# Optimization experiments

Measured on AMD Instinct MI355X. Metric: run time of the kernel, lower is better.

The kernel has to match this reference:

```python
import jax, jax.numpy as jnp
import numpy as np

N = 100000          # item_nums (nodes)
E = 3200000         # edges
D = 64              # embedding dim
MASK_DEPTH = 2      # configs['model']['mask_depth']
PATH_PROB = 0.5     # configs['model']['path_prob']
NUM_CAND = 1024     # configs['model']['num_mask_cand']
EPS_DIV = 1e-8
EPS_NORM = 1e-12


def setup_inputs() -> dict:
    key = jax.random.key(0)
    k1, k2, k3, k4 = jax.random.split(key, 4)
    edge_rows = jax.random.randint(k1, (E,), 0, N, dtype=jnp.int32)
    edge_cols = jax.random.randint(k2, (E,), 0, N, dtype=jnp.int32)
    edge_vals = jax.random.uniform(k3, (E,), dtype=jnp.float32)
    embeds = jax.random.normal(k4, (N, D), dtype=jnp.float32)
    return {"edge_rows": edge_rows, "edge_cols": edge_cols,
            "edge_vals": edge_vals, "embeds": embeds}


def _l2norm(x):
    # torch F.normalize(p=2, dim=1)
    n = jnp.sqrt(jnp.sum(x * x, axis=-1, keepdims=True))
    return x / jnp.maximum(n, EPS_NORM)


def reference(edge_rows, edge_cols, edge_vals, embeds):
    def spmm(vals, x):  # adj @ x with adj in COO form; x: [N, d]
        return jax.ops.segment_sum(vals[:, None] * x[edge_cols], edge_rows,
                                   num_segments=N)

    def rowsum(vals):   # t.sparse.sum(adj, dim=-1) -> [N, 1]
        return jax.ops.segment_sum(vals, edge_rows, num_segments=N)[:, None]

    key = jax.random.key(42)
    vals = edge_vals

    order = rowsum(vals)
    fst = spmm(vals, embeds) - embeds            # fstEmbeds
    emb_sum, num_sum = fst, order                # running sum of emb/num lists
    emb_prev, num_prev = fst, order

    for i in range(MASK_DEPTH):
        key, kd = jax.random.split(key)
        keep = PATH_PROB ** (i + 1)
        # sparse_dropout: keep edge with prob `keep`, values NOT rescaled.
        # Dropping edges == zeroing their values for all subsequent spmm.
        mask = jnp.floor(jax.random.uniform(kd, (E,)) + keep)
        vals = vals * mask
        emb_new = spmm(vals, emb_prev) - emb_prev - order * emb_prev
        num_new = spmm(vals, num_prev) - num_prev - order
        order = rowsum(vals)
        emb_sum = emb_sum + emb_new
        num_sum = num_sum + num_new
        emb_prev, num_prev = emb_new, num_new

    subgraph = _l2norm(emb_sum / (num_sum + EPS_DIV))
    embeds_n = _l2norm(embeds)
    scores = jnp.sum(subgraph * embeds_n, axis=-1)   # [N]

    # make_noise: Gumbel noise -log(-log(U))
    key, kn = jax.random.split(key)
    u = jax.random.uniform(kn, (N,))
    scores = scores + (-jnp.log(-jnp.log(u)))

    _, candidates = jax.lax.top_k(scores, NUM_CAND)
    return scores, candidates
```

## Files before the change

kernel.cpp:

```cpp
#include <hip/hip_runtime.h>
#include <hip/hip_bf16.h>
#include <stdint.h>
#include <stddef.h>

#define NN 100000
#define NE 3200000
#define NCAND 1024
#define SCAN_BLOCKS 98
#define NB 391
#define CAP 10240
#define TILE 4096
#define NA_CAP 1700000
#define NB_CAP 500000

__host__ __device__ inline void tf2x32(uint32_t k0, uint32_t k1,
                                       uint32_t x0, uint32_t x1,
                                       uint32_t& y0, uint32_t& y1) {
  uint32_t ks2 = k0 ^ k1 ^ 0x1BD11BDAu;
  x0 += k0; x1 += k1;
#define TFR(r) { x0 += x1; x1 = (x1 << (r)) | (x1 >> (32 - (r))); x1 ^= x0; }
  TFR(13) TFR(15) TFR(26) TFR(6)
  x0 += k1;  x1 += ks2 + 1u;
  TFR(17) TFR(29) TFR(16) TFR(24)
  x0 += ks2; x1 += k0 + 2u;
  TFR(13) TFR(15) TFR(26) TFR(6)
  x0 += k0;  x1 += k1 + 3u;
  TFR(17) TFR(29) TFR(16) TFR(24)
  x0 += k1;  x1 += ks2 + 4u;
  TFR(13) TFR(15) TFR(26) TFR(6)
  x0 += ks2; x1 += k0 + 5u;
#undef TFR
  y0 = x0; y1 = x1;
}

__device__ inline float u01_from_key(uint32_t ka, uint32_t kb, uint32_t idx) {
  uint32_t y0, y1; tf2x32(ka, kb, 0u, idx, y0, y1);
  uint32_t bits = y0 ^ y1;
  return __uint_as_float((bits >> 9) | 0x3F800000u) - 1.0f;
}

__device__ inline float np_tree64(float w) {
#pragma clang fp contract(off)
  float acc = w;
  acc = acc + __shfl_down(w, 8);
  acc = acc + __shfl_down(w, 16);
  acc = acc + __shfl_down(w, 24);
  acc = acc + __shfl_down(w, 32);
  acc = acc + __shfl_down(w, 40);
  acc = acc + __shfl_down(w, 48);
  acc = acc + __shfl_down(w, 56);
  float u = acc + __shfl_xor(acc, 1);
  float v = u + __shfl_xor(u, 2);
  float f = v + __shfl_xor(v, 4);
  return __shfl(f, 0);
}

__global__ void __launch_bounds__(256) k_bucketA(const int* __restrict__ rows,
    const int* __restrict__ cols, const float* __restrict__ vals,
    uint32_t* __restrict__ bcur, uint32_t* __restrict__ bbufE,
    uint32_t* __restrict__ bbufC, float* __restrict__ bbufV,
    uint32_t kd0a, uint32_t kd0b, uint32_t kd1a, uint32_t kd1b) {
  __shared__ uint32_t cnt[NB], cnt2[NB], gbase[NB];
  __shared__ uint32_t pref[NB + 1];
  __shared__ uint32_t stageE[TILE];
  __shared__ uint32_t stageC[TILE];
  __shared__ float    stageV[TILE];
  __shared__ uint16_t stageB[TILE];
  int tid = threadIdx.x;
  int base_e = blockIdx.x * TILE;
  int vcnt = NE - base_e; if (vcnt > TILE) vcnt = TILE;
  for (int j = tid; j < NB; j += 256) { cnt[j] = 0u; cnt2[j] = 0u; }
  __syncthreads();
  for (int i = tid; i < vcnt; i += 256) {
    uint32_t r = (uint32_t)rows[base_e + i];
    atomicAdd(&cnt[r >> 8], 1u);
  }
  __syncthreads();
  if (tid == 0) {
    uint32_t run = 0;
    for (int j = 0; j < NB; j++) { pref[j] = run; run += cnt[j]; }
    pref[NB] = run;
  }
  for (int j = tid; j < NB; j += 256) gbase[j] = atomicAdd(&bcur[j], cnt[j]);
  __syncthreads();
  for (int i = tid; i < vcnt; i += 256) {
    uint32_t e = (uint32_t)(base_e + i);
    uint32_t r = (uint32_t)rows[e];
    uint32_t b = r >> 8, lr = r & 255u;
    uint32_t m0 = (u01_from_key(kd0a, kd0b, e) >= 0.5f) ? 1u : 0u;
    uint32_t m1 = (u01_from_key(kd1a, kd1b, e) >= 0.75f) ? 1u : 0u;
    uint32_t flags = (m0 << 30) | ((m0 & m1) << 31);
    uint32_t slot = pref[b] + atomicAdd(&cnt2[b], 1u);
    stageE[slot] = flags | (lr << 22) | e;
    stageC[slot] = (uint32_t)cols[e];
    stageV[slot] = vals[e];
    stageB[slot] = (uint16_t)b;
  }
  __syncthreads();
  for (int i = tid; i < vcnt; i += 256) {
    uint32_t b = stageB[i];
    size_t dst = (size_t)b * CAP + gbase[b] + ((uint32_t)i - pref[b]);
    bbufE[dst] = stageE[i];
    bbufC[dst] = stageC[i];
    bbufV[dst] = stageV[i];
  }
}

__global__ void __launch_bounds__(256) k_cnt(const uint32_t* __restrict__ bcur,
    const uint32_t* __restrict__ bbufE, uint32_t* __restrict__ total,
    uint32_t* __restrict__ totalA, uint32_t* __restrict__ totalB) {
  __shared__ uint32_t c0[256], c1[256], c2[256];
  int b = blockIdx.x, tid = threadIdx.x;
  c0[tid] = 0u; c1[tid] = 0u; c2[tid] = 0u;
  __syncthreads();
  uint32_t nE = bcur[b];
  for (uint32_t i = tid; i < nE; i += 256) {
    uint32_t pk = bbufE[(size_t)b * CAP + i];
    uint32_t lr = (pk >> 22) & 255u;
    atomicAdd(&c0[lr], 1u);
    if (pk & 0x40000000u) atomicAdd(&c1[lr], 1u);
    if (pk & 0x80000000u) atomicAdd(&c2[lr], 1u);
  }
  __syncthreads();
  int row = (b << 8) + tid;
  if (row < NN) { total[row] = c0[tid]; totalA[row] = c1[tid]; totalB[row] = c2[tid]; }
}

__global__ void k_scan1(const uint32_t* __restrict__ total, uint32_t* __restrict__ rstart,
                        uint32_t* __restrict__ bsum) {
  __shared__ uint32_t s[1024];
  int i = blockIdx.x * 1024 + threadIdx.x;
  uint32_t v = (i < NN) ? total[i] : 0u;
  s[threadIdx.x] = v; __syncthreads();
  for (int o = 1; o < 1024; o <<= 1) {
    uint32_t x = (threadIdx.x >= (unsigned)o) ? s[threadIdx.x - o] : 0u;
    __syncthreads();
    s[threadIdx.x] += x;
    __syncthreads();
  }
  if (i <= NN) rstart[i] = s[threadIdx.x] - v;
  if (threadIdx.x == 1023) bsum[blockIdx.x] = s[1023];
}

__global__ void k_scan2(uint32_t* __restrict__ bsum) {
  if (blockIdx.x == 0 && threadIdx.x == 0) {
    uint32_t run = 0;
    for (int b = 0; b < SCAN_BLOCKS; b++) { uint32_t t = bsum[b]; bsum[b] = run; run += t; }
  }
}

__global__ void k_scan3(uint32_t* __restrict__ rstart, const uint32_t* __restrict__ bsum) {
  int i = blockIdx.x * 1024 + threadIdx.x;
  if (i <= NN) rstart[i] += bsum[blockIdx.x];
}

__global__ void __launch_bounds__(256) k_buildB(const uint32_t* __restrict__ bbufE,
    const uint32_t* __restrict__ bbufC, const float* __restrict__ bbufV,
    const uint32_t* __restrict__ rstart, const uint32_t* __restrict__ rstartA,
    const uint32_t* __restrict__ rstartB,
    uint32_t* __restrict__ scol, float* __restrict__ v0s,
    uint32_t* __restrict__ scolA, float* __restrict__ vAa,
    uint32_t* __restrict__ scolB, float* __restrict__ vBa,
    float* __restrict__ order0, float* __restrict__ order1) {
#pragma clang fp contract(off)
  __shared__ uint32_t eidp[CAP];
  __shared__ uint16_t slot[CAP];
  __shared__ uint32_t rbase[257];
  __shared__ uint32_t rcur[256];
  int b = blockIdx.x, tid = threadIdx.x;
  int row0 = b << 8;
  int nrows = NN - row0; if (nrows > 256) nrows = 256;
  uint32_t base = rstart[row0];
  for (int j = tid; j <= nrows; j += 256) rbase[j] = rstart[row0 + j] - base;
  rcur[tid] = 0u;
  __syncthreads();
  uint32_t nE = rbase[nrows];
  const uint32_t* bE = bbufE + (size_t)b * CAP;
  const uint32_t* bC = bbufC + (size_t)b * CAP;
  const float*    bV = bbufV + (size_t)b * CAP;
  for (uint32_t i = tid; i < nE; i += 256) {
    uint32_t pk = bE[i];
    uint32_t lr = (pk >> 22) & 255u;
    uint32_t c = atomicAdd(&rcur[lr], 1u);
    uint32_t pos = rbase[lr] + c;
    eidp[pos] = pk;
    slot[pos] = (uint16_t)i;
  }
  __syncthreads();
  for (int lr = tid; lr < nrows; lr += 256) {
    uint32_t p0 = rbase[lr], p1 = rbase[lr + 1];
    for (uint32_t i = p0 + 1; i < p1; i++) {
      uint32_t key = eidp[i]; uint16_t ks = slot[i];
      uint32_t ke = key & 0x3FFFFFu;
      uint32_t j = i;
      while (j > p0 && (eidp[j - 1] & 0x3FFFFFu) > ke) {
        eidp[j] = eidp[j - 1]; slot[j] = slot[j - 1]; j--;
      }
      eidp[j] = key; slot[j] = ks;
    }
  }
  __syncthreads();
  for (uint32_t i = tid; i < nE; i += 256) {
    uint32_t s = slot[i];
    scol[(size_t)base + i] = bC[s];
    v0s[(size_t)base + i] = bV[s];
  }
  for (int lr = tid; lr < nrows; lr += 256) {
    uint32_t p0 = rbase[lr], p1 = rbase[lr + 1];
    uint32_t wA = rstartA[row0 + lr];
    uint32_t wB = rstartB[row0 + lr];
    float o0 = 0.0f, o1 = 0.0f;
    for (uint32_t p = p0; p < p1; p++) {
      uint32_t pk = eidp[p];
      uint32_t s = slot[p];
      float v = bV[s];
      o0 = o0 + v;
      if (pk & 0x40000000u) {
        o1 = o1 + v;
        uint32_t c = bC[s];
        scolA[wA] = c; vAa[wA] = v; wA++;
        if (pk & 0x80000000u) { scolB[wB] = c; vBa[wB] = v; wB++; }
      }
    }
    order0[row0 + lr] = o0; order1[row0 + lr] = o1;
  }
}

__global__ void __launch_bounds__(256) k_fst(const uint32_t* __restrict__ rp,
    const uint32_t* __restrict__ scol, const float* __restrict__ v0s,
    const float* __restrict__ emb, float* __restrict__ fst) {
#pragma clang fp contract(off)
  int r = blockIdx.x * 4 + (threadIdx.x >> 6);
  if (r >= NN) return;
  int d = threadIdx.x & 63;
  uint32_t p0 = rp[r], p1 = rp[r + 1];
  float acc = 0.0f;
  uint32_t p = p0;
  for (; p + 4 <= p1; p += 4) {
    uint32_t c0 = scol[p], c1 = scol[p + 1], c2 = scol[p + 2], c3 = scol[p + 3];
    float v0 = v0s[p], v1 = v0s[p + 1], v2 = v0s[p + 2], v3 = v0s[p + 3];
    float e0 = emb[(size_t)c0 * 64 + d];
    float e1 = emb[(size_t)c1 * 64 + d];
    float e2 = emb[(size_t)c2 * 64 + d];
    float e3 = emb[(size_t)c3 * 64 + d];
    acc = acc + v0 * e0; acc = acc + v1 * e1;
    acc = acc + v2 * e2; acc = acc + v3 * e3;
  }
  for (; p < p1; p++) acc = acc + v0s[p] * emb[(size_t)scol[p] * 64 + d];
  fst[(size_t)r * 64 + d] = acc - emb[(size_t)r * 64 + d];
}

__global__ void __launch_bounds__(256) k_numA(const uint32_t* __restrict__ rpA,
    const uint32_t* __restrict__ scolA, const float* __restrict__ vAa,
    const float* __restrict__ order0, float* __restrict__ num0) {
#pragma clang fp contract(off)
  int r = blockIdx.x * blockDim.x + threadIdx.x;
  if (r >= NN) return;
  uint32_t p0 = rpA[r], p1 = rpA[r + 1];
  float acc = 0.0f;
  uint32_t p = p0;
  for (; p + 4 <= p1; p += 4) {
    uint32_t c0 = scolA[p], c1 = scolA[p + 1], c2 = scolA[p + 2], c3 = scolA[p + 3];
    float v0 = vAa[p], v1 = vAa[p + 1], v2 = vAa[p + 2], v3 = vAa[p + 3];
    float o0 = order0[c0], o1 = order0[c1], o2 = order0[c2], o3 = order0[c3];
    acc = acc + v0 * o0; acc = acc + v1 * o1;
    acc = acc + v2 * o2; acc = acc + v3 * o3;
  }
  for (; p < p1; p++) acc = acc + vAa[p] * order0[scolA[p]];
  float o = order0[r];
  num0[r] = (acc - o) - o;
}

__global__ void __launch_bounds__(256) k_emb1(const uint32_t* __restrict__ rpA,
    const uint32_t* __restrict__ scolA, const float* __restrict__ vAa,
    const float* __restrict__ fst, const float* __restrict__ order0,
    float* __restrict__ emb1) {
#pragma clang fp contract(off)
  int r = blockIdx.x * 4 + (threadIdx.x >> 6);
  if (r >= NN) return;
  int d = threadIdx.x & 63;
  uint32_t p0 = rpA[r], p1 = rpA[r + 1];
  float acc = 0.0f;
  uint32_t p = p0;
  for (; p + 4 <= p1; p += 4) {
    uint32_t c0 = scolA[p], c1 = scolA[p + 1], c2 = scolA[p + 2], c3 = scolA[p + 3];
    float v0 = vAa[p], v1 = vAa[p + 1], v2 = vAa[p + 2], v3 = vAa[p + 3];
    float e0 = fst[(size_t)c0 * 64 + d];
    float e1 = fst[(size_t)c1 * 64 + d];
    float e2 = fst[(size_t)c2 * 64 + d];
    float e3 = fst[(size_t)c3 * 64 + d];
    acc = acc + v0 * e0; acc = acc + v1 * e1;
    acc = acc + v2 * e2; acc = acc + v3 * e3;
  }
  for (; p < p1; p++) acc = acc + vAa[p] * fst[(size_t)scolA[p] * 64 + d];
  size_t i = (size_t)r * 64 + d;
  float pr = fst[i];
  float t  = order0[r] * pr;
  emb1[i] = (acc - pr) - t;
}

__global__ void __launch_bounds__(256) k_numB(const uint32_t* __restrict__ rpB,
    const uint32_t* __restrict__ scolB, const float* __restrict__ vBa,
    const float* __restrict__ num0, const float* __restrict__ order0,
    const float* __restrict__ order1, float* __restrict__ num_sum) {
#pragma clang fp contract(off)
  int r = blockIdx.x * blockDim.x + threadIdx.x;
  if (r >= NN) return;
  uint32_t p0 = rpB[r], p1 = rpB[r + 1];
  float acc = 0.0f;
  for (uint32_t p = p0; p < p1; p++) acc = acc + vBa[p] * num0[scolB[p]];
  float n1 = (acc - num0[r]) - order1[r];
  num_sum[r] = (order0[r] + num0[r]) + n1;
}

__global__ void __launch_bounds__(256) k_emb2(const uint32_t* __restrict__ rpB,
    const uint32_t* __restrict__ scolB, const float* __restrict__ vBa,
    const float* __restrict__ emb1, const float* __restrict__ order1,
    float* __restrict__ fstsum) {
#pragma clang fp contract(off)
  int r = blockIdx.x * 4 + (threadIdx.x >> 6);
  if (r >= NN) return;
  int d = threadIdx.x & 63;
  uint32_t p0 = rpB[r], p1 = rpB[r + 1];
  float acc = 0.0f;
  uint32_t p = p0;
  for (; p + 4 <= p1; p += 4) {
    uint32_t c0 = scolB[p], c1 = scolB[p + 1], c2 = scolB[p + 2], c3 = scolB[p + 3];
    float v0 = vBa[p], v1 = vBa[p + 1], v2 = vBa[p + 2], v3 = vBa[p + 3];
    float e0 = emb1[(size_t)c0 * 64 + d];
    float e1 = emb1[(size_t)c1 * 64 + d];
    float e2 = emb1[(size_t)c2 * 64 + d];
    float e3 = emb1[(size_t)c3 * 64 + d];
    acc = acc + v0 * e0; acc = acc + v1 * e1;
    acc = acc + v2 * e2; acc = acc + v3 * e3;
  }
  for (; p < p1; p++) acc = acc + vBa[p] * emb1[(size_t)scolB[p] * 64 + d];
  size_t i = (size_t)r * 64 + d;
  float pr = emb1[i];
  float t  = order1[r] * pr;
  float e2v = (acc - pr) - t;
  fstsum[i] = (fstsum[i] + pr) + e2v;
}

__global__ void __launch_bounds__(256) k_scores(const float* __restrict__ esum,
    const float* __restrict__ num_sum, const float* __restrict__ emb,
    uint32_t* __restrict__ m_arr, float* __restrict__ out_scores,
    uint32_t kna, uint32_t knb) {
#pragma clang fp contract(off)
  int r = blockIdx.x * 4 + (threadIdx.x >> 6);
  if (r >= NN) return;
  int lane = threadIdx.x & 63;
  size_t ib = (size_t)r * 64 + lane;
  float denom = num_sum[r] + 1e-8f;
  float t = esum[ib] / denom;
  float S1 = np_tree64(t * t);
  float nn = fmaxf(sqrtf(S1), 1e-12f);
  t = t / nn;
  float e = emb[ib];
  float S2 = np_tree64(e * e);
  float mn = fmaxf(sqrtf(S2), 1e-12f);
  float s = np_tree64(t * (e / mn));
  if (lane == 0) {
    float u  = u01_from_key(kna, knb, (uint32_t)r);
    float l1 = (float)log((double)u);
    float l2 = (float)log((double)(-l1));
    s = s + (-l2);
    uint32_t bb = __float_as_uint(s);
    m_arr[r] = bb ^ (uint32_t)(((int32_t)bb >> 31) | (int32_t)0x80000000);
    out_scores[r] = s;
  }
}

__global__ void __launch_bounds__(1024)
k_topk(const uint32_t* __restrict__ m_arr, float* __restrict__ out) {
  __shared__ uint32_t hist[256];
  __shared__ uint32_t selp, need, ccnt;
  __shared__ unsigned long long cbuf[4096];
  int tid = threadIdx.x;
  if (tid == 0) { selp = 0u; need = NCAND; ccnt = 0u; }
  __syncthreads();
  for (int shift = 24; shift >= 0; shift -= 8) {
    if (tid < 256) hist[tid] = 0u;
    __syncthreads();
    uint32_t pref = selp;
    for (int i = tid; i < NN; i += 1024) {
      uint32_t m = m_arr[i];
      bool ok = (shift == 24) || ((m >> (shift + 8)) == pref);
      if (ok) atomicAdd(&hist[(m >> shift) & 255u], 1u);
    }
    __syncthreads();
    if (tid == 0) {
      uint32_t nd = need;
      int b;
      for (b = 255; b > 0; b--) {
        uint32_t c = hist[b];
        if (c < nd) nd -= c; else break;
      }
      selp = (pref << 8) | (uint32_t)b;
      need = nd;
    }
    __syncthreads();
  }
  uint32_t thr = selp;
  for (int i = tid; i < NN; i += 1024) {
    uint32_t m = m_arr[i];
    if (m >= thr) {
      uint32_t pos = atomicAdd(&ccnt, 1u);
      if (pos < 4096u)
        cbuf[pos] = ((unsigned long long)m << 32) | (uint32_t)(~(uint32_t)i);
    }
  }
  __syncthreads();
  uint32_t n = ccnt; if (n > 4096u) n = 4096u;
  for (int i = tid; i < 4096; i += 1024) if (i >= (int)n) cbuf[i] = 0ULL;
  __syncthreads();
  for (int k = 2; k <= 4096; k <<= 1) {
    for (int j = k >> 1; j > 0; j >>= 1) {
      for (int i = tid; i < 4096; i += 1024) {
        int ixj = i ^ j;
        if (ixj > i) {
          bool up = ((i & k) == 0);
          unsigned long long a = cbuf[i], b = cbuf[ixj];
          if ((a > b) == up) { cbuf[i] = b; cbuf[ixj] = a; }
        }
      }
      __syncthreads();
    }
  }
  for (int j = tid; j < NCAND; j += 1024) {
    unsigned long long key = cbuf[4095 - j];
    uint32_t idx = ~(uint32_t)(key & 0xFFFFFFFFull);
    out[j] = (float)idx;
  }
}

extern "C" void kernel_launch(void* const* d_in, const int* in_sizes, int n_in,
                              void* d_out, int out_size, void* d_ws, size_t ws_size,
                              hipStream_t stream) {
  (void)in_sizes; (void)n_in; (void)out_size; (void)ws_size;
  const int*   rows = (const int*)d_in[0];
  const int*   cols = (const int*)d_in[1];
  const float* vals = (const float*)d_in[2];
  const float* emb  = (const float*)d_in[3];
  float* out = (float*)d_out;

  char* w = (char*)d_ws;
  auto alloc = [&](size_t bytes) -> void* {
    void* p = (void*)w; w += (bytes + 255) & ~(size_t)255; return p;
  };
  uint32_t* bcur    = (uint32_t*)alloc((size_t)NB * 4);
  uint32_t* bbufE   = (uint32_t*)alloc((size_t)NB * CAP * 4);
  uint32_t* bbufC   = (uint32_t*)alloc((size_t)NB * CAP * 4);
  float*    bbufV   = (float*)   alloc((size_t)NB * CAP * 4);
  uint32_t* total   = (uint32_t*)alloc((size_t)NN * 4);
  uint32_t* totalA  = (uint32_t*)alloc((size_t)NN * 4);
  uint32_t* totalB  = (uint32_t*)alloc((size_t)NN * 4);
  uint32_t* rstart  = (uint32_t*)alloc((size_t)(NN + 1) * 4);
  uint32_t* rstartA = (uint32_t*)alloc((size_t)(NN + 1) * 4);
  uint32_t* rstartB = (uint32_t*)alloc((size_t)(NN + 1) * 4);
  uint32_t* bsum    = (uint32_t*)alloc((size_t)SCAN_BLOCKS * 4);
  uint32_t* scol    = (uint32_t*)alloc((size_t)NE * 4);
  float*    v0s     = (float*)   alloc((size_t)NE * 4);
  uint32_t* scolA   = (uint32_t*)alloc((size_t)NA_CAP * 4);
  float*    vAa     = (float*)   alloc((size_t)NA_CAP * 4);
  uint32_t* scolB   = (uint32_t*)alloc((size_t)NB_CAP * 4);
  float*    vBa     = (float*)   alloc((size_t)NB_CAP * 4);
  float*    order0  = (float*)   alloc((size_t)NN * 4);
  float*    order1  = (float*)   alloc((size_t)NN * 4);
  float*    num0    = (float*)   alloc((size_t)NN * 4);
  float*    num_sum = (float*)   alloc((size_t)NN * 4);
  float*    fst     = (float*)   alloc((size_t)NN * 64 * 4);
  float*    emb1    = (float*)   alloc((size_t)NN * 64 * 4);
  uint32_t* m_arr   = (uint32_t*)alloc((size_t)NN * 4);

  uint32_t K1a,K1b, kd0a,kd0b, K2a,K2b, kd1a,kd1b, kna,knb;
  tf2x32(0u, 42u, 0u, 0u, K1a, K1b);
  tf2x32(0u, 42u, 0u, 1u, kd0a, kd0b);
  tf2x32(K1a, K1b, 0u, 0u, K2a, K2b);
  tf2x32(K1a, K1b, 0u, 1u, kd1a, kd1b);
  tf2x32(K2a, K2b, 0u, 1u, kna, knb);

  hipMemsetAsync(bcur, 0, (size_t)NB * 4, stream);

  const int TPB = 256;
  k_bucketA<<<(NE + TILE - 1) / TILE, TPB, 0, stream>>>(rows, cols, vals, bcur,
      bbufE, bbufC, bbufV, kd0a, kd0b, kd1a, kd1b);
  k_cnt<<<NB, TPB, 0, stream>>>(bcur, bbufE, total, totalA, totalB);
  k_scan1<<<SCAN_BLOCKS, 1024, 0, stream>>>(total, rstart, bsum);
  k_scan2<<<1, 1, 0, stream>>>(bsum);
  k_scan3<<<SCAN_BLOCKS, 1024, 0, stream>>>(rstart, bsum);
  k_scan1<<<SCAN_BLOCKS, 1024, 0, stream>>>(totalA, rstartA, bsum);
  k_scan2<<<1, 1, 0, stream>>>(bsum);
  k_scan3<<<SCAN_BLOCKS, 1024, 0, stream>>>(rstartA, bsum);
  k_scan1<<<SCAN_BLOCKS, 1024, 0, stream>>>(totalB, rstartB, bsum);
  k_scan2<<<1, 1, 0, stream>>>(bsum);
  k_scan3<<<SCAN_BLOCKS, 1024, 0, stream>>>(rstartB, bsum);
  k_buildB<<<NB, TPB, 0, stream>>>(bbufE, bbufC, bbufV, rstart, rstartA, rstartB,
      scol, v0s, scolA, vAa, scolB, vBa, order0, order1);
  k_fst<<<(NN + 3) / 4, TPB, 0, stream>>>(rstart, scol, v0s, emb, fst);
  k_numA<<<(NN + TPB - 1) / TPB, TPB, 0, stream>>>(rstartA, scolA, vAa, order0, num0);
  k_emb1<<<(NN + 3) / 4, TPB, 0, stream>>>(rstartA, scolA, vAa, fst, order0, emb1);
  k_numB<<<(NN + TPB - 1) / TPB, TPB, 0, stream>>>(rstartB, scolB, vBa, num0, order0, order1, num_sum);
  k_emb2<<<(NN + 3) / 4, TPB, 0, stream>>>(rstartB, scolB, vBa, emb1, order1, fst);
  k_scores<<<(NN + 3) / 4, TPB, 0, stream>>>(fst, num_sum, emb, m_arr, out, kna, knb);
  k_topk<<<1, 1024, 0, stream>>>(m_arr, out + NN);
}
```

Before: 833.5 us.

## Split single-block radix top-k into multi-block histogram, select, collect, sort kernels

Replaces the single-block top-k, which made four radix passes over all scores with one workgroup, with a pipeline. A grid-wide 16-bit histogram uses global atomics, one block picks the threshold bin, a multi-block collect gathers candidates above it, and one block bitonic-sorts them. The goal is to spread the full passes over the score array across many CUs instead of one. In exchange it adds kernel launches, two memsets, contention on the global histogram atomics, and a coarser threshold that could admit more candidates than the 4096-entry buffer holds.

```diff
diff --git a/kernel.cpp b/kernel.cpp
--- a/kernel.cpp
+++ b/kernel.cpp
@@ -12,6 +12,7 @@
 #define TILE 4096
 #define NA_CAP 1700000
 #define NB_CAP 500000
+#define HBINS 65536
 
 __host__ __device__ inline void tf2x32(uint32_t k0, uint32_t k1,
                                        uint32_t x0, uint32_t x1,
@@ -371,48 +372,60 @@
   }
 }
 
-__global__ void __launch_bounds__(1024)
-k_topk(const uint32_t* __restrict__ m_arr, float* __restrict__ out) {
-  __shared__ uint32_t hist[256];
-  __shared__ uint32_t selp, need, ccnt;
-  __shared__ unsigned long long cbuf[4096];
-  int tid = threadIdx.x;
-  if (tid == 0) { selp = 0u; need = NCAND; ccnt = 0u; }
-  __syncthreads();
-  for (int shift = 24; shift >= 0; shift -= 8) {
-    if (tid < 256) hist[tid] = 0u;
-    __syncthreads();
-    uint32_t pref = selp;
-    for (int i = tid; i < NN; i += 1024) {
-      uint32_t m = m_arr[i];
-      bool ok = (shift == 24) || ((m >> (shift + 8)) == pref);
-      if (ok) atomicAdd(&hist[(m >> shift) & 255u], 1u);
+__global__ void __launch_bounds__(1024) k_h16(const uint32_t* __restrict__ m_arr,
+                                              uint32_t* __restrict__ hist16) {
+  int i = blockIdx.x * 1024 + threadIdx.x;
+  if (i < NN) atomicAdd(&hist16[m_arr[i] >> 16], 1u);
+}
+
+__global__ void __launch_bounds__(1024) k_sel16(const uint32_t* __restrict__ hist16,
+                                                uint32_t* __restrict__ selthr) {
+  __shared__ uint32_t part[1024];
+  int t = threadIdx.x;
+  uint32_t s = 0;
+  for (int j = 0; j < 64; j++) s += hist16[t * 64 + j];
+  part[t] = s;
+  __syncthreads();
+  if (t == 0) {
+    uint32_t acc = 0;
+    int c = 1023;
+    for (; c >= 0; c--) {
+      if (acc + part[c] >= (uint32_t)NCAND) break;
+      acc += part[c];
     }
-    __syncthreads();
-    if (tid == 0) {
-      uint32_t nd = need;
-      int b;
-      for (b = 255; b > 0; b--) {
-        uint32_t c = hist[b];
-        if (c < nd) nd -= c; else break;
-      }
-      selp = (pref << 8) | (uint32_t)b;
-      need = nd;
+    uint32_t thr = 0;
+    if (c >= 0) {
+      int b = c * 64 + 63;
+      for (; b >= c * 64; b--) { acc += hist16[b]; if (acc >= (uint32_t)NCAND) break; }
+      thr = (uint32_t)b << 16;
     }
-    __syncthreads();
-  }
-  uint32_t thr = selp;
-  for (int i = tid; i < NN; i += 1024) {
+    selthr[0] = thr;
+  }
+}
+
+__global__ void __launch_bounds__(256) k_collect(const uint32_t* __restrict__ m_arr,
+    const uint32_t* __restrict__ selthr, unsigned long long* __restrict__ cbuf,
+    uint32_t* __restrict__ ccnt) {
+  int i = blockIdx.x * blockDim.x + threadIdx.x;
+  int stride = gridDim.x * blockDim.x;
+  uint32_t thr = selthr[0];
+  for (; i < NN; i += stride) {
     uint32_t m = m_arr[i];
     if (m >= thr) {
-      uint32_t pos = atomicAdd(&ccnt, 1u);
+      uint32_t pos = atomicAdd(ccnt, 1u);
       if (pos < 4096u)
         cbuf[pos] = ((unsigned long long)m << 32) | (uint32_t)(~(uint32_t)i);
     }
   }
-  __syncthreads();
-  uint32_t n = ccnt; if (n > 4096u) n = 4096u;
-  for (int i = tid; i < 4096; i += 1024) if (i >= (int)n) cbuf[i] = 0ULL;
+}
+
+__global__ void __launch_bounds__(1024) k_sortemit(
+    const unsigned long long* __restrict__ gcbuf, const uint32_t* __restrict__ ccnt,
+    float* __restrict__ out) {
+  __shared__ unsigned long long cbuf[4096];
+  int tid = threadIdx.x;
+  uint32_t n = *ccnt; if (n > 4096u) n = 4096u;
+  for (int i = tid; i < 4096; i += 1024) cbuf[i] = (i < (int)n) ? gcbuf[i] : 0ULL;
   __syncthreads();
   for (int k = 2; k <= 4096; k <<= 1) {
     for (int j = k >> 1; j > 0; j >>= 1) {
@@ -472,6 +485,10 @@
   float*    fst     = (float*)   alloc((size_t)NN * 64 * 4);
   float*    emb1    = (float*)   alloc((size_t)NN * 64 * 4);
   uint32_t* m_arr   = (uint32_t*)alloc((size_t)NN * 4);
+  uint32_t* hist16  = (uint32_t*)alloc((size_t)HBINS * 4);
+  uint32_t* selthr  = (uint32_t*)alloc(4);
+  uint32_t* gccnt   = (uint32_t*)alloc(4);
+  unsigned long long* gcbuf = (unsigned long long*)alloc(4096 * 8);
 
   uint32_t K1a,K1b, kd0a,kd0b, K2a,K2b, kd1a,kd1b, kna,knb;
   tf2x32(0u, 42u, 0u, 0u, K1a, K1b);
@@ -481,6 +498,8 @@
   tf2x32(K2a, K2b, 0u, 1u, kna, knb);
 
   hipMemsetAsync(bcur, 0, (size_t)NB * 4, stream);
+  hipMemsetAsync(hist16, 0, (size_t)HBINS * 4, stream);
+  hipMemsetAsync(gccnt, 0, 4, stream);
 
   const int TPB = 256;
   k_bucketA<<<(NE + TILE - 1) / TILE, TPB, 0, stream>>>(rows, cols, vals, bcur,
@@ -503,5 +522,8 @@
   k_numB<<<(NN + TPB - 1) / TPB, TPB, 0, stream>>>(rstartB, scolB, vBa, num0, order0, order1, num_sum);
   k_emb2<<<(NN + 3) / 4, TPB, 0, stream>>>(rstartB, scolB, vBa, emb1, order1, fst);
   k_scores<<<(NN + 3) / 4, TPB, 0, stream>>>(fst, num_sum, emb, m_arr, out, kna, knb);
-  k_topk<<<1, 1024, 0, stream>>>(m_arr, out + NN);
-}
+  k_h16<<<(NN + 1023) / 1024, 1024, 0, stream>>>(m_arr, hist16);
+  k_sel16<<<1, 1024, 0, stream>>>(hist16, selthr);
+  k_collect<<<64, TPB, 0, stream>>>(m_arr, selthr, gcbuf, gccnt);
+  k_sortemit<<<1, 1024, 0, stream>>>(gcbuf, gccnt, out + NN);
+}
```

After: 811.0 us. 1.03x faster.
